# Performance work log

Measured on AMD Instinct MI355X. Metric: run time of the kernel, lower is better.

## Reference

```python
import jax, jax.numpy as jnp
import numpy as np

L, B, H, Y, C = 256, 256, 256, 32, 16  # seq len, batch, hidden, y_size, spline channels (u_size+1)


def setup_inputs() -> dict:
    key = jax.random.key(0)
    ks = jax.random.split(key, 10)
    # times: uniform grid 0..L-1 (torchcde default spline parameterization), shape (L,B,1)
    ts = jnp.broadcast_to(jnp.arange(L, dtype=jnp.float32)[:, None, None], (L, B, 1))
    us = jax.random.normal(ks[0], (L, B, C - 1), dtype=jnp.float32)
    h0 = 0.1 * jax.random.normal(ks[1], (B, H), dtype=jnp.float32)
    s = 1.0 / np.sqrt(H)
    # NCDEFunc: Linear(H,H) -> relu -> Linear(H, H*C) -> tanh -> view(B,H,C)
    W1 = jax.random.uniform(ks[2], (H, H), jnp.float32, -s, s)
    b1 = jax.random.uniform(ks[3], (H,), jnp.float32, -s, s)
    W2 = jax.random.uniform(ks[4], (H, H * C), jnp.float32, -s, s)
    b2 = jax.random.uniform(ks[5], (H * C,), jnp.float32, -s, s)
    # decoder MLP(H, 2H, Y, 1): Linear(H,2H) -> tanh -> Linear(2H,Y)
    dW1 = jax.random.uniform(ks[6], (H, 2 * H), jnp.float32, -s, s)
    db1 = jax.random.uniform(ks[7], (2 * H,), jnp.float32, -s, s)
    s2 = 1.0 / np.sqrt(2 * H)
    dW2 = jax.random.uniform(ks[8], (2 * H, Y), jnp.float32, -s2, s2)
    db2 = jax.random.uniform(ks[9], (Y,), jnp.float32, -s2, s2)
    return dict(ts=ts, us=us, h0=h0, W1=W1, b1=b1, W2=W2, b2=b2,
                dW1=dW1, db1=db1, dW2=dW2, db2=db2)


def reference(ts, us, h0, W1, b1, W2, b2, dW1, db1, dW2, db2):
    # permute to batch-first and build control path x: (B, L, C)
    xb = jnp.concatenate([jnp.transpose(ts, (1, 0, 2)), jnp.transpose(us, (1, 0, 2))], axis=2)
    # hermite cubic with backward differences on unit grid (torchcde default t=arange):
    # node derivative d_i = x_i - x_{i-1} (delta=1); d_0 = d_1
    diffs = xb[:, 1:] - xb[:, :-1]                      # (B, L-1, C)
    dnode = jnp.concatenate([diffs[:, :1], diffs], axis=1)  # (B, L, C)
    t = ts[:, 0, 0]  # (L,) -- cdeint t grid = ts.squeeze(-1)[0,:] after permute

    def dXdt(s_):
        # derivative of the hermite cubic spline at scalar time s_ (unit knot spacing)
        idx = jnp.clip(jnp.floor(s_).astype(jnp.int32), 0, L - 2)
        tau = s_ - idx.astype(s_.dtype)
        xi, xip = xb[:, idx], xb[:, idx + 1]            # (B, C)
        di, dip = dnode[:, idx], dnode[:, idx + 1]
        h00p = 6.0 * tau * tau - 6.0 * tau              # h01' = -h00'
        h10p = 3.0 * tau * tau - 4.0 * tau + 1.0
        h11p = 3.0 * tau * tau - 2.0 * tau
        return h00p * (xi - xip) + h10p * di + h11p * dip  # (B, C)

    def vf(z):
        # NCDEFunc: z (B,H) -> matrix (B,H,C)
        hid = jax.nn.relu(z @ W1 + b1)
        return jnp.tanh(hid @ W2 + b2).reshape(B, H, C)

    def step(z, inp):
        s_, dt_ = inp
        dz = jnp.einsum('bhc,bc->bh', vf(z), dXdt(s_))  # f(z) @ dX/dt
        zn = z + dt_ * dz                               # Euler update on grid t
        return zn, zn

    _, zs = jax.lax.scan(step, h0, (t[:-1], t[1:] - t[:-1]))
    z_seq = jnp.concatenate([h0[None], zs], axis=0)     # (L, B, H): cdeint output at all t
    # decoder then permute(1,0,2) -> already time-major here: (L, B, Y)
    return jnp.tanh(z_seq @ dW1 + db1) @ dW2 + db2
```

## Files before the change

### kernel.cpp

```cpp
#include <hip/hip_runtime.h>
#include <math.h>

#define LL 256
#define BB 256
#define HH 256
#define CC 16
#define YY 32
#define HC (HH*CC)
#define NSTEP (LL-1)
#define NBG 32
#define BGB 8
#define HCH 32
#define TPB 1024
#define NJS 8
#define AJS 16

__device__ __forceinline__ float fast_tanh(float x) {
    float e = __expf(2.0f * x);
    return 1.0f - 2.0f / (e + 1.0f);
}

__device__ __forceinline__ float2 ld_coh2(const float* p) {
    union { unsigned long long u; float2 f; } cv;
    cv.u = __hip_atomic_load((const unsigned long long*)p,
                             __ATOMIC_RELAXED, __HIP_MEMORY_SCOPE_AGENT);
    return cv.f;
}
__device__ __forceinline__ void st_coh(float* p, float v) {
    __hip_atomic_store(p, v, __ATOMIC_RELAXED, __HIP_MEMORY_SCOPE_AGENT);
}

__device__ __forceinline__ void bg_barrier(unsigned* cnt, unsigned target) {
    __syncthreads();
    if (threadIdx.x == 0) {
        __hip_atomic_fetch_add(cnt, 1u, __ATOMIC_RELAXED, __HIP_MEMORY_SCOPE_AGENT);
        while (__hip_atomic_load(cnt, __ATOMIC_RELAXED, __HIP_MEMORY_SCOPE_AGENT) < target)
            __builtin_amdgcn_s_sleep(2);
    }
    __syncthreads();
}

__global__ void __launch_bounds__(TPB)
k_scan(const float* __restrict__ us, const float* __restrict__ W1,
       const float* __restrict__ b1, const float* __restrict__ W2,
       const float* __restrict__ b2, float* __restrict__ zs,
       unsigned* __restrict__ barG) {
    __shared__ float smem[NJS * BGB * 512 + 2048 + 2048 + 512 + 128 + 256];
    float* psum  = smem;
    float* pa    = smem;
    float* z_loc = smem + NJS * BGB * 512;
    float* hidT  = z_loc + BGB * HH;
    float* b2s   = hidT + HH * BGB;
    float* dvs   = b2s + 512;
    float* b1s   = dvs + 128;

    const int bg = blockIdx.x >> 3;
    const int hc = blockIdx.x & 7;
    const int t  = threadIdx.x;
    const int b0 = bg * BGB;
    const int n0 = hc * HCH * CC;

    for (int i = t; i < 512; i += TPB) b2s[i] = b2[n0 + i];
    for (int i = t; i < HH; i += TPB) b1s[i] = b1[i];
    __syncthreads();

    unsigned* cnt = barG + (size_t)bg * 64;

    const int sb  = t >> 7;
    const int sj2 = (t & 127) << 1;
    const int hq  = t & 63;
    const int ajs = t >> 6;
    const int jsp = t >> 7;
    const int ct  = (t & 127) << 2;
    const int col = t & 511;
    const int bh  = (t >> 9) << 2;

    for (int k = 0; k < NSTEP; k++) {
        const size_t zk = (size_t)k * (BB * HH);

        {
            float2 v = ld_coh2(&zs[zk + (size_t)(b0 + sb) * HH + sj2]);
            *(float2*)&z_loc[sb * HH + sj2] = v;
        }
        if (t < BGB * CC) {
            int b = t >> 4, c = t & 15;
            int kk = (k < 1) ? 1 : k;
            float v = 1.0f;
            if (c > 0)
                v = us[((size_t)kk * BB + b0 + b) * (CC - 1) + c - 1]
                  - us[((size_t)(kk - 1) * BB + b0 + b) * (CC - 1) + c - 1];
            dvs[b * CC + c] = v;
        }
        __syncthreads();

        {
            float4 accA[BGB];
            #pragma unroll
            for (int b = 0; b < BGB; b++) accA[b] = make_float4(0.f, 0.f, 0.f, 0.f);
            const float* w1p = &W1[(size_t)(ajs * 16) * HH + hq * 4];
            #pragma unroll 4
            for (int j = 0; j < 16; j++) {
                float4 w = *(const float4*)&w1p[(size_t)j * HH];
                #pragma unroll
                for (int b = 0; b < BGB; b++) {
                    float zv = z_loc[b * HH + ajs * 16 + j];
                    accA[b].x += zv * w.x; accA[b].y += zv * w.y;
                    accA[b].z += zv * w.z; accA[b].w += zv * w.w;
                }
            }
            #pragma unroll
            for (int b = 0; b < BGB; b++)
                *(float4*)&pa[ajs * 2048 + b * 256 + hq * 4] = accA[b];
        }
        __syncthreads();
        {
            #pragma unroll
            for (int rep = 0; rep < 2; rep++) {
                int o = t + rep * 1024;
                float s = b1s[o & 255];
                #pragma unroll
                for (int q = 0; q < AJS; q++) s += pa[q * 2048 + o];
                hidT[(o & 255) * BGB + (o >> 8)] = fmaxf(s, 0.f);
            }
        }
        __syncthreads();

        {
            float4 acc[BGB];
            #pragma unroll
            for (int b = 0; b < BGB; b++) acc[b] = make_float4(0.f, 0.f, 0.f, 0.f);
            const int jb = jsp * 32;
            const float* w2p = &W2[(size_t)jb * HC + n0 + ct];
            #pragma unroll 4
            for (int j = 0; j < 32; j++) {
                float4 hA = *(const float4*)&hidT[(jb + j) * BGB];
                float4 hB = *(const float4*)&hidT[(jb + j) * BGB + 4];
                float4 w  = *(const float4*)&w2p[(size_t)j * HC];
                acc[0].x += hA.x * w.x; acc[0].y += hA.x * w.y;
                acc[0].z += hA.x * w.z; acc[0].w += hA.x * w.w;
                acc[1].x += hA.y * w.x; acc[1].y += hA.y * w.y;
                acc[1].z += hA.y * w.z; acc[1].w += hA.y * w.w;
                acc[2].x += hA.z * w.x; acc[2].y += hA.z * w.y;
                acc[2].z += hA.z * w.z; acc[2].w += hA.z * w.w;
                acc[3].x += hA.w * w.x; acc[3].y += hA.w * w.y;
                acc[3].z += hA.w * w.z; acc[3].w += hA.w * w.w;
                acc[4].x += hB.x * w.x; acc[4].y += hB.x * w.y;
                acc[4].z += hB.x * w.z; acc[4].w += hB.x * w.w;
                acc[5].x += hB.y * w.x; acc[5].y += hB.y * w.y;
                acc[5].z += hB.y * w.z; acc[5].w += hB.y * w.w;
                acc[6].x += hB.z * w.x; acc[6].y += hB.z * w.y;
                acc[6].z += hB.z * w.z; acc[6].w += hB.z * w.w;
                acc[7].x += hB.w * w.x; acc[7].y += hB.w * w.y;
                acc[7].z += hB.w * w.z; acc[7].w += hB.w * w.w;
            }
            #pragma unroll
            for (int b = 0; b < BGB; b++)
                *(float4*)&psum[((jsp * BGB + b) << 9) + ct] = acc[b];
        }
        __syncthreads();

        {
            #pragma unroll
            for (int q = 0; q < 4; q++) {
                int b = bh + q;
                float g = b2s[col];
                #pragma unroll
                for (int s = 0; s < NJS; s++)
                    g += psum[((s * BGB + b) << 9) + col];
                float v = fast_tanh(g) * dvs[b * CC + (col & 15)];
                v += __shfl_xor(v, 1);
                v += __shfl_xor(v, 2);
                v += __shfl_xor(v, 4);
                v += __shfl_xor(v, 8);
                if ((col & 15) == 0) {
                    int hl = col >> 4;
                    int h = hc * HCH + hl;
                    st_coh(&zs[zk + (size_t)(BB * HH) + (size_t)(b0 + b) * HH + h],
                           z_loc[b * HH + h] + v);
                }
            }
        }
        bg_barrier(cnt, 8u * (unsigned)(k + 1));
    }
}

__global__ void k_out(const float* __restrict__ zseq, const float* __restrict__ dW1,
                      const float* __restrict__ db1, const float* __restrict__ dW2,
                      const float* __restrict__ db2, float* __restrict__ out) {
    __shared__ float zt[16][HH];
    __shared__ float act[16][2 * HH];
    int r0 = blockIdx.x * 16;
    int t  = threadIdx.x;
    {
        const float4* src = (const float4*)(zseq + (size_t)r0 * HH);
        float4* dst = (float4*)&zt[0][0];
        for (int i = t; i < 1024; i += 256) dst[i] = src[i];
    }
    __syncthreads();
    {
        int c0  = (t & 127) * 4;
        int rr0 = (t >> 7) * 8;
        float a[8][4];
        #pragma unroll
        for (int i = 0; i < 8; i++)
            #pragma unroll
            for (int q = 0; q < 4; q++) a[i][q] = 0.f;
        for (int j = 0; j < HH; j++) {
            float4 w = *(const float4*)&dW1[(size_t)j * 2 * HH + c0];
            #pragma unroll
            for (int i = 0; i < 8; i++) {
                float zv = zt[rr0 + i][j];
                a[i][0] += zv * w.x; a[i][1] += zv * w.y;
                a[i][2] += zv * w.z; a[i][3] += zv * w.w;
            }
        }
        float4 bias = *(const float4*)&db1[c0];
        #pragma unroll
        for (int i = 0; i < 8; i++) {
            act[rr0 + i][c0 + 0] = fast_tanh(a[i][0] + bias.x);
            act[rr0 + i][c0 + 1] = fast_tanh(a[i][1] + bias.y);
            act[rr0 + i][c0 + 2] = fast_tanh(a[i][2] + bias.z);
            act[rr0 + i][c0 + 3] = fast_tanh(a[i][3] + bias.w);
        }
    }
    __syncthreads();
    {
        int rl = t >> 4;
        int y2 = t & 15;
        float o0 = 0.f, o1 = 0.f;
        #pragma unroll 4
        for (int j = 0; j < 2 * HH; j++) {
            float av = act[rl][j];
            float2 w = *(const float2*)&dW2[(size_t)j * YY + y2 * 2];
            o0 += av * w.x; o1 += av * w.y;
        }
        float2 bias = *(const float2*)&db2[y2 * 2];
        out[(size_t)(r0 + rl) * YY + y2 * 2]     = o0 + bias.x;
        out[(size_t)(r0 + rl) * YY + y2 * 2 + 1] = o1 + bias.y;
    }
}

extern "C" void kernel_launch(void* const* d_in, const int* in_sizes, int n_in,
                              void* d_out, int out_size, void* d_ws, size_t ws_size,
                              hipStream_t stream) {
    const float* us  = (const float*)d_in[1];
    const float* h0  = (const float*)d_in[2];
    const float* W1  = (const float*)d_in[3];
    const float* b1  = (const float*)d_in[4];
    const float* W2  = (const float*)d_in[5];
    const float* b2  = (const float*)d_in[6];
    const float* dW1 = (const float*)d_in[7];
    const float* db1 = (const float*)d_in[8];
    const float* dW2 = (const float*)d_in[9];
    const float* db2 = (const float*)d_in[10];
    float* out = (float*)d_out;

    float* zs   = (float*)d_ws;
    unsigned* barG = (unsigned*)(zs + (size_t)LL * BB * HH);

    hipMemcpyAsync(zs, h0, (size_t)BB * HH * sizeof(float),
                   hipMemcpyDeviceToDevice, stream);
    hipMemsetAsync(barG, 0, NBG * 64 * sizeof(unsigned), stream);

    k_scan<<<NBG * 8, TPB, 0, stream>>>(us, W1, b1, W2, b2, zs, barG);
    k_out<<<LL * BB / 16, 256, 0, stream>>>(zs, dW1, db1, dW2, db2, out);
}
```

Measured before the change: 4.231 ms.

## Split first-layer matmul across blocks with global hidden exchange and 16-batch groups

Changes the scan work partition from 32 batch groups of 8 with 8 column-chunk blocks to 16 batch groups of 16 with 16 column-slice blocks. The first layer is no longer computed redundantly by every block: each block computes 16 hidden units from a transposed W1 slice cached in shared memory and publishes them through a global exchange buffer. This adds a second group barrier per step. Each W2 element loaded is now reused across 16 batch rows instead of 8, and the barrier now uses release/acquire ordering. Precise tanhf replaces the fast tanh approximation, which costs more per element.

```diff
diff --git a/kernel.cpp b/kernel.cpp
--- a/kernel.cpp
+++ b/kernel.cpp
@@ -8,12 +8,10 @@
 #define YY 32
 #define HC (HH*CC)
 #define NSTEP (LL-1)
-#define NBG 32
-#define BGB 8
-#define HCH 32
 #define TPB 1024
-#define NJS 8
-#define AJS 16
+#define NG 16
+#define GB 16
+#define NSL 16
 
 __device__ __forceinline__ float fast_tanh(float x) {
     float e = __expf(2.0f * x);
@@ -33,8 +31,8 @@
 __device__ __forceinline__ void bg_barrier(unsigned* cnt, unsigned target) {
     __syncthreads();
     if (threadIdx.x == 0) {
-        __hip_atomic_fetch_add(cnt, 1u, __ATOMIC_RELAXED, __HIP_MEMORY_SCOPE_AGENT);
-        while (__hip_atomic_load(cnt, __ATOMIC_RELAXED, __HIP_MEMORY_SCOPE_AGENT) < target)
+        __hip_atomic_fetch_add(cnt, 1u, __ATOMIC_RELEASE, __HIP_MEMORY_SCOPE_AGENT);
+        while (__hip_atomic_load(cnt, __ATOMIC_ACQUIRE, __HIP_MEMORY_SCOPE_AGENT) < target)
             __builtin_amdgcn_s_sleep(2);
     }
     __syncthreads();
@@ -44,143 +42,138 @@
 k_scan(const float* __restrict__ us, const float* __restrict__ W1,
        const float* __restrict__ b1, const float* __restrict__ W2,
        const float* __restrict__ b2, float* __restrict__ zs,
-       unsigned* __restrict__ barG) {
-    __shared__ float smem[NJS * BGB * 512 + 2048 + 2048 + 512 + 128 + 256];
+       float* __restrict__ hidX, unsigned* __restrict__ barG) {
+    __shared__ float smem[4*GB*256 + GB*260 + 4096 + 16*260 + 256 + 256 + 16];
     float* psum  = smem;
     float* pa    = smem;
-    float* z_loc = smem + NJS * BGB * 512;
-    float* hidT  = z_loc + BGB * HH;
-    float* b2s   = hidT + HH * BGB;
-    float* dvs   = b2s + 512;
-    float* b1s   = dvs + 128;
-
-    const int bg = blockIdx.x >> 3;
-    const int hc = blockIdx.x & 7;
+    float* z_locB= smem + 4*GB*256;
+    float* hidT  = z_locB + GB*260;
+    float* w1sT  = hidT + 4096;
+    float* b2s   = w1sT + 16*260;
+    float* dvs   = b2s + 256;
+    float* b1s   = dvs + 256;
+
     const int t  = threadIdx.x;
-    const int b0 = bg * BGB;
-    const int n0 = hc * HCH * CC;
-
-    for (int i = t; i < 512; i += TPB) b2s[i] = b2[n0 + i];
-    for (int i = t; i < HH; i += TPB) b1s[i] = b1[i];
-    __syncthreads();
-
-    unsigned* cnt = barG + (size_t)bg * 64;
-
-    const int sb  = t >> 7;
-    const int sj2 = (t & 127) << 1;
-    const int hq  = t & 63;
-    const int ajs = t >> 6;
-    const int jsp = t >> 7;
-    const int ct  = (t & 127) << 2;
-    const int col = t & 511;
-    const int bh  = (t >> 9) << 2;
+    const int bg = blockIdx.x >> 4;
+    const int sl = blockIdx.x & 15;
+    const int b0 = bg * GB;
+    const int n0 = sl * 256;
+    unsigned* cnt = barG + bg * 64;
+
+    for (int i = t; i < 16 * 256; i += TPB) {
+        int hl = i >> 8, j = i & 255;
+        w1sT[hl * 260 + j] = W1[(size_t)j * HH + sl * 16 + hl];
+    }
+    for (int i = t; i < 256; i += TPB) b2s[i] = b2[n0 + i];
+    if (t < 16) b1s[t] = b1[sl * 16 + t];
+    __syncthreads();
+
+    const int o   = t & 255;
+    const int jq  = t >> 8;
+    const int col = t & 255;
+    const int bq0 = (t >> 8) << 2;
 
     for (int k = 0; k < NSTEP; k++) {
         const size_t zk = (size_t)k * (BB * HH);
 
-        {
-            float2 v = ld_coh2(&zs[zk + (size_t)(b0 + sb) * HH + sj2]);
-            *(float2*)&z_loc[sb * HH + sj2] = v;
-        }
-        if (t < BGB * CC) {
+        #pragma unroll
+        for (int rep = 0; rep < 2; rep++) {
+            int p = t + rep * 1024;
+            int b = p >> 7, off = (p & 127) << 1;
+            float2 v = ld_coh2(&zs[zk + (size_t)(b0 + b) * HH + off]);
+            *(float2*)&z_locB[b * 260 + off] = v;
+        }
+        if (t < GB * CC) {
             int b = t >> 4, c = t & 15;
             int kk = (k < 1) ? 1 : k;
             float v = 1.0f;
             if (c > 0)
                 v = us[((size_t)kk * BB + b0 + b) * (CC - 1) + c - 1]
                   - us[((size_t)(kk - 1) * BB + b0 + b) * (CC - 1) + c - 1];
-            dvs[b * CC + c] = v;
+            dvs[t] = v;
         }
         __syncthreads();
 
         {
-            float4 accA[BGB];
-            #pragma unroll
-            for (int b = 0; b < BGB; b++) accA[b] = make_float4(0.f, 0.f, 0.f, 0.f);
-            const float* w1p = &W1[(size_t)(ajs * 16) * HH + hq * 4];
+            const int ha = o >> 4, ba = o & 15;
+            const float* wp = &w1sT[ha * 260 + jq * 64];
+            const float* zp = &z_locB[ba * 260 + jq * 64];
+            float acc = 0.f;
+            #pragma unroll
+            for (int j4 = 0; j4 < 64; j4 += 4) {
+                float4 w = *(const float4*)&wp[j4];
+                float4 z = *(const float4*)&zp[j4];
+                acc += w.x * z.x + w.y * z.y + w.z * z.z + w.w * z.w;
+            }
+            pa[jq * 256 + o] = acc;
+        }
+        __syncthreads();
+        if (t < 256) {
+            int ha = t >> 4, ba = t & 15;
+            float s = (pa[t] + pa[256 + t]) + (pa[512 + t] + pa[768 + t])
+                    + b1s[ha];
+            st_coh(&hidX[bg * 4096 + (sl * 16 + ha) * 16 + ba], fmaxf(s, 0.f));
+        }
+        bg_barrier(cnt, 16u * (2u * (unsigned)k + 1u));
+
+        #pragma unroll
+        for (int rep = 0; rep < 2; rep++) {
+            int p = t + rep * 1024;
+            float2 v = ld_coh2(&hidX[bg * 4096 + (p << 1)]);
+            *(float2*)&hidT[p << 1] = v;
+        }
+        __syncthreads();
+
+        {
+            float acc[GB];
+            #pragma unroll
+            for (int b = 0; b < GB; b++) acc[b] = 0.f;
+            const float* w2p = &W2[(size_t)(jq * 64) * HC + n0 + col];
+            const float* hp  = &hidT[(jq * 64) * GB];
             #pragma unroll 4
-            for (int j = 0; j < 16; j++) {
-                float4 w = *(const float4*)&w1p[(size_t)j * HH];
-                #pragma unroll
-                for (int b = 0; b < BGB; b++) {
-                    float zv = z_loc[b * HH + ajs * 16 + j];
-                    accA[b].x += zv * w.x; accA[b].y += zv * w.y;
-                    accA[b].z += zv * w.z; accA[b].w += zv * w.w;
-                }
-            }
-            #pragma unroll
-            for (int b = 0; b < BGB; b++)
-                *(float4*)&pa[ajs * 2048 + b * 256 + hq * 4] = accA[b];
-        }
-        __syncthreads();
+            for (int j = 0; j < 64; j++) {
+                float w  = w2p[(size_t)j * HC];
+                float4 hA = *(const float4*)&hp[j * GB];
+                float4 hB = *(const float4*)&hp[j * GB + 4];
+                float4 hC = *(const float4*)&hp[j * GB + 8];
+                float4 hD = *(const float4*)&hp[j * GB + 12];
+                acc[0]  += hA.x * w; acc[1]  += hA.y * w;
+                acc[2]  += hA.z * w; acc[3]  += hA.w * w;
+                acc[4]  += hB.x * w; acc[5]  += hB.y * w;
+                acc[6]  += hB.z * w; acc[7]  += hB.w * w;
+                acc[8]  += hC.x * w; acc[9]  += hC.y * w;
+                acc[10] += hC.z * w; acc[11] += hC.w * w;
+                acc[12] += hD.x * w; acc[13] += hD.y * w;
+                acc[14] += hD.z * w; acc[15] += hD.w * w;
+            }
+            #pragma unroll
+            for (int b = 0; b < GB; b++)
+                psum[(jq * GB + b) * 256 + col] = acc[b];
+        }
+        __syncthreads();
+
         {
             #pragma unroll
-            for (int rep = 0; rep < 2; rep++) {
-                int o = t + rep * 1024;
-                float s = b1s[o & 255];
-                #pragma unroll
-                for (int q = 0; q < AJS; q++) s += pa[q * 2048 + o];
-                hidT[(o & 255) * BGB + (o >> 8)] = fmaxf(s, 0.f);
-            }
-        }
-        __syncthreads();
-
-        {
-            float4 acc[BGB];
-            #pragma unroll
-            for (int b = 0; b < BGB; b++) acc[b] = make_float4(0.f, 0.f, 0.f, 0.f);
-            const int jb = jsp * 32;
-            const float* w2p = &W2[(size_t)jb * HC + n0 + ct];
-            #pragma unroll 4
-            for (int j = 0; j < 32; j++) {
-                float4 hA = *(const float4*)&hidT[(jb + j) * BGB];
-                float4 hB = *(const float4*)&hidT[(jb + j) * BGB + 4];
-                float4 w  = *(const float4*)&w2p[(size_t)j * HC];
-                acc[0].x += hA.x * w.x; acc[0].y += hA.x * w.y;
-                acc[0].z += hA.x * w.z; acc[0].w += hA.x * w.w;
-                acc[1].x += hA.y * w.x; acc[1].y += hA.y * w.y;
-                acc[1].z += hA.y * w.z; acc[1].w += hA.y * w.w;
-                acc[2].x += hA.z * w.x; acc[2].y += hA.z * w.y;
-                acc[2].z += hA.z * w.z; acc[2].w += hA.z * w.w;
-                acc[3].x += hA.w * w.x; acc[3].y += hA.w * w.y;
-                acc[3].z += hA.w * w.z; acc[3].w += hA.w * w.w;
-                acc[4].x += hB.x * w.x; acc[4].y += hB.x * w.y;
-                acc[4].z += hB.x * w.z; acc[4].w += hB.x * w.w;
-                acc[5].x += hB.y * w.x; acc[5].y += hB.y * w.y;
-                acc[5].z += hB.y * w.z; acc[5].w += hB.y * w.w;
-                acc[6].x += hB.z * w.x; acc[6].y += hB.z * w.y;
-                acc[6].z += hB.z * w.z; acc[6].w += hB.z * w.w;
-                acc[7].x += hB.w * w.x; acc[7].y += hB.w * w.y;
-                acc[7].z += hB.w * w.z; acc[7].w += hB.w * w.w;
-            }
-            #pragma unroll
-            for (int b = 0; b < BGB; b++)
-                *(float4*)&psum[((jsp * BGB + b) << 9) + ct] = acc[b];
-        }
-        __syncthreads();
-
-        {
-            #pragma unroll
             for (int q = 0; q < 4; q++) {
-                int b = bh + q;
-                float g = b2s[col];
-                #pragma unroll
-                for (int s = 0; s < NJS; s++)
-                    g += psum[((s * BGB + b) << 9) + col];
-                float v = fast_tanh(g) * dvs[b * CC + (col & 15)];
+                int b = bq0 + q;
+                float g = (psum[(0 * GB + b) * 256 + col]
+                         + psum[(1 * GB + b) * 256 + col])
+                        + (psum[(2 * GB + b) * 256 + col]
+                         + psum[(3 * GB + b) * 256 + col]);
+                g += b2s[col];
+                float v = tanhf(g) * dvs[b * CC + (col & 15)];
                 v += __shfl_xor(v, 1);
                 v += __shfl_xor(v, 2);
                 v += __shfl_xor(v, 4);
                 v += __shfl_xor(v, 8);
                 if ((col & 15) == 0) {
-                    int hl = col >> 4;
-                    int h = hc * HCH + hl;
-                    st_coh(&zs[zk + (size_t)(BB * HH) + (size_t)(b0 + b) * HH + h],
-                           z_loc[b * HH + h] + v);
+                    int hg = sl * 16 + (col >> 4);
+                    st_coh(&zs[zk + (size_t)(BB * HH) + (size_t)(b0 + b) * HH + hg],
+                           z_locB[b * 260 + hg] + v);
                 }
             }
         }
-        bg_barrier(cnt, 8u * (unsigned)(k + 1));
+        bg_barrier(cnt, 16u * (2u * (unsigned)k + 2u));
     }
 }
 
@@ -256,12 +249,13 @@
     float* out = (float*)d_out;
 
     float* zs   = (float*)d_ws;
-    unsigned* barG = (unsigned*)(zs + (size_t)LL * BB * HH);
+    float* hidX = zs + (size_t)LL * BB * HH;
+    unsigned* barG = (unsigned*)(hidX + NG * 4096);
 
     hipMemcpyAsync(zs, h0, (size_t)BB * HH * sizeof(float),
                    hipMemcpyDeviceToDevice, stream);
-    hipMemsetAsync(barG, 0, NBG * 64 * sizeof(unsigned), stream);
-
-    k_scan<<<NBG * 8, TPB, 0, stream>>>(us, W1, b1, W2, b2, zs, barG);
+    hipMemsetAsync(barG, 0, NG * 64 * sizeof(unsigned), stream);
+
+    k_scan<<<NG * NSL, TPB, 0, stream>>>(us, W1, b1, W2, b2, zs, hidX, barG);
     k_out<<<LL * BB / 16, 256, 0, stream>>>(zs, dW1, db1, dW2, db2, out);
 }
```

Measured after the change: 7.124 ms. 68.4% more time.
